# Optimization experiments

Measured on AMD Instinct MI355X. Metric: run time of the kernel, lower is better.

## Reference

```python
import jax, jax.numpy as jnp
import numpy as np

B, C, H, W = 32, 64, 128, 128
RADIUS = 30


def _dw(x, w, dil, pad):
    # depthwise conv, NCHW, groups = C
    return jax.lax.conv_general_dilated(
        x, w, window_strides=(1, 1), padding=[(pad, pad), (pad, pad)],
        rhs_dilation=(dil, dil),
        dimension_numbers=('NCHW', 'OIHW', 'NCHW'),
        feature_group_count=x.shape[1])


def _pw(x, w):
    # 1x1 conv: w is [out_ch, in_ch]
    return jnp.einsum('bchw,oc->bohw', x, w)


def _aff(x, s, b):
    # folded BatchNorm (inference): per-channel scale + bias
    return x * s[None, :, None, None] + b[None, :, None, None]


def setup_inputs() -> dict:
    key = jax.random.key(0)
    ks = iter(jax.random.split(key, 40))
    nk = lambda: next(ks)
    rn = lambda shape, sc=0.1: jax.random.normal(nk(), shape, jnp.float32) * sc
    ru = lambda shape: jax.random.uniform(nk(), shape, jnp.float32, minval=0.5, maxval=1.5)
    d = {'x': jax.random.normal(nk(), (B, C, H, W), jnp.float32)}
    d['dws_dw'] = rn((C, 1, 3, 3)); d['dws_s1'] = ru((C,)); d['dws_b1'] = rn((C,))
    d['dws_pw'] = rn((C, C)); d['dws_s2'] = ru((C,)); d['dws_b2'] = rn((C,))
    kern = {1: 1, 2: 3, 3: 3, 4: 3}
    for i in (1, 2, 3, 4):
        d[f'dw{i}_w'] = rn((C, 1, kern[i], kern[i]))
        d[f'dw{i}_s'] = ru((C,)); d[f'dw{i}_b'] = rn((C,))
        d[f'pw{i}_w'] = rn((C // 4, C)); d[f'pw{i}_s'] = ru((C // 4,)); d[f'pw{i}_b'] = rn((C // 4,))
    d['conv_w'] = rn((1, C)); d['conv_s'] = ru((1,)); d['conv_b'] = rn((1,))
    d['radius'] = RADIUS
    return d


def reference(x, dws_dw, dws_s1, dws_b1, dws_pw, dws_s2, dws_b2,
              dw1_w, dw1_s, dw1_b, pw1_w, pw1_s, pw1_b,
              dw2_w, dw2_s, dw2_b, pw2_w, pw2_s, pw2_b,
              dw3_w, dw3_s, dw3_b, pw3_w, pw3_s, pw3_b,
              dw4_w, dw4_s, dw4_b, pw4_w, pw4_s, pw4_b,
              conv_w, conv_s, conv_b, radius):
    rows, cols = x.shape[-2], x.shape[-1]
    # vectorized radial mask (original builds this with a Python double loop)
    ii = jnp.arange(rows, dtype=jnp.float32)[:, None]
    jj = jnp.arange(cols, dtype=jnp.float32)[None, :]
    dis = jnp.sqrt((ii - rows / 2) ** 2 + (jj - rows / 2) ** 2)  # note: imageSize=rows for both axes, as in original
    mask = (dis < radius).astype(x.dtype)
    # FFT high-pass filter
    xf = jnp.fft.fftshift(jnp.fft.fft2(x, axes=(-2, -1)), axes=(-2, -1))
    hf = xf * (1.0 - mask)
    x_h = jnp.abs(jnp.fft.ifft2(jnp.fft.ifftshift(hf, axes=(-2, -1)), axes=(-2, -1))).astype(x.dtype)
    # DWSConv: depthwise 3x3 + BN + ReLU, then pointwise + BN + ReLU
    e = jax.nn.relu(_aff(_dw(x_h, dws_dw, 1, 1), dws_s1, dws_b1))
    e = jax.nn.relu(_aff(_pw(e, dws_pw), dws_s2, dws_b2))
    skip = e

    def branch(t, dw_w, dw_s, dw_b, pw_w, pw_s, pw_b, dil, pad):
        # DWConv (depthwise + BN + ReLU) then BasicConv2d 1x1 (conv + BN)
        t = jax.nn.relu(_aff(_dw(t, dw_w, dil, pad), dw_s, dw_b))
        return _aff(_pw(t, pw_w), pw_s, pw_b)

    em = jnp.concatenate([
        branch(e, dw1_w, dw1_s, dw1_b, pw1_w, pw1_s, pw1_b, 1, 0),
        branch(e, dw2_w, dw2_s, dw2_b, pw2_w, pw2_s, pw2_b, 1, 1),
        branch(e, dw3_w, dw3_s, dw3_b, pw3_w, pw3_s, pw3_b, 3, 3),
        branch(e, dw4_w, dw4_s, dw4_b, pw4_w, pw4_s, pw4_b, 5, 5),
    ], axis=1) + skip
    edge = jax.nn.relu(_aff(_pw(em, conv_w), conv_s, conv_b))  # [B,1,H,W]
    return _aff(_pw(x + edge, conv_w), conv_s, conv_b)  # shared self.conv applied again
```

## Files before the change

### kernel.cpp

```cpp
#include <hip/hip_runtime.h>


__device__ __forceinline__ float2 cmul(float2 a, float2 b) {
  return make_float2(a.x * b.x - a.y * b.y, a.x * b.y + a.y * b.x);
}
__device__ __forceinline__ float2 cadd(float2 a, float2 b) {
  return make_float2(a.x + b.x, a.y + b.y);
}
__device__ __forceinline__ float2 csub(float2 a, float2 b) {
  return make_float2(a.x - b.x, a.y - b.y);
}
__device__ __forceinline__ float2 conjf2(float2 a) {
  return make_float2(a.x, -a.y);
}

__device__ __forceinline__ void gload16(const float* g, void* l) {
  __builtin_amdgcn_global_load_lds(
      (const __attribute__((address_space(1))) void*)g,
      (__attribute__((address_space(3))) void*)l, 16, 0, 0);
}

__device__ __forceinline__ int swz(int r, int c) {
  return (r << 7) | (c ^ (r & 31));
}

__device__ __forceinline__ void bf3_fwd(float2 x[8], float2 t0, float2 t1,
                                        float2 t2, float2 t3, float2 tp0,
                                        float2 tp1, float2 tpp) {
  float2 y0 = cadd(x[0], x[4]), y4 = cmul(csub(x[0], x[4]), t0);
  float2 y1 = cadd(x[1], x[5]), y5 = cmul(csub(x[1], x[5]), t1);
  float2 y2 = cadd(x[2], x[6]), y6 = cmul(csub(x[2], x[6]), t2);
  float2 y3 = cadd(x[3], x[7]), y7 = cmul(csub(x[3], x[7]), t3);
  float2 z0 = cadd(y0, y2), z2 = cmul(csub(y0, y2), tp0);
  float2 z1 = cadd(y1, y3), z3 = cmul(csub(y1, y3), tp1);
  float2 z4 = cadd(y4, y6), z6 = cmul(csub(y4, y6), tp0);
  float2 z5 = cadd(y5, y7), z7 = cmul(csub(y5, y7), tp1);
  x[0] = cadd(z0, z1); x[1] = cmul(csub(z0, z1), tpp);
  x[2] = cadd(z2, z3); x[3] = cmul(csub(z2, z3), tpp);
  x[4] = cadd(z4, z5); x[5] = cmul(csub(z4, z5), tpp);
  x[6] = cadd(z6, z7); x[7] = cmul(csub(z6, z7), tpp);
}

__device__ __forceinline__ void bf3_inv(float2 x[8], float2 w0, float2 w10,
                                        float2 w11, float2 w20, float2 w21,
                                        float2 w22, float2 w23) {
  float2 t;
  t = cmul(x[1], w0); float2 y0 = cadd(x[0], t), y1 = csub(x[0], t);
  t = cmul(x[3], w0); float2 y2 = cadd(x[2], t), y3 = csub(x[2], t);
  t = cmul(x[5], w0); float2 y4 = cadd(x[4], t), y5 = csub(x[4], t);
  t = cmul(x[7], w0); float2 y6 = cadd(x[6], t), y7 = csub(x[6], t);
  t = cmul(y2, w10); float2 z0 = cadd(y0, t), z2 = csub(y0, t);
  t = cmul(y3, w11); float2 z1 = cadd(y1, t), z3 = csub(y1, t);
  t = cmul(y6, w10); float2 z4 = cadd(y4, t), z6 = csub(y4, t);
  t = cmul(y7, w11); float2 z5 = cadd(y5, t), z7 = csub(y5, t);
  t = cmul(z4, w20); x[0] = cadd(z0, t); x[4] = csub(z0, t);
  t = cmul(z5, w21); x[1] = cadd(z1, t); x[5] = csub(z1, t);
  t = cmul(z6, w22); x[2] = cadd(z2, t); x[6] = csub(z2, t);
  t = cmul(z7, w23); x[3] = cadd(z3, t); x[7] = csub(z3, t);
}

template <bool COL, int S>
__device__ __forceinline__ void fwd_tri(float2* img, const float2* tw,
                                        int tid) {
  constexpr int m4 = 1 << (S - 2);
#pragma unroll
  for (int k = 0; k < 2; ++k) {
    int g = tid + (k << 10);
    int line = COL ? (g & 127) : (g >> 4);
    int gidx = COL ? (g >> 7) : (g & 15);
    int q = gidx >> (S - 2);
    int j = gidx & (m4 - 1);
    int off0 = (q << (S + 1)) + j;
    int ad[8];
    float2 x[8];
#pragma unroll
    for (int i = 0; i < 8; ++i) {
      int el = off0 + i * m4;
      ad[i] = COL ? swz(el, line) : swz(line, el);
      x[i] = img[ad[i]];
    }
    bf3_fwd(x, tw[j << (6 - S)], tw[(j + m4) << (6 - S)],
            tw[(j + 2 * m4) << (6 - S)], tw[(j + 3 * m4) << (6 - S)],
            tw[j << (7 - S)], tw[(j + m4) << (7 - S)], tw[j << (8 - S)]);
#pragma unroll
    for (int i = 0; i < 8; ++i) img[ad[i]] = x[i];
  }
  __syncthreads();
}

__device__ __forceinline__ void fwd_rows6_g(const float* __restrict__ p0,
                                            const float* __restrict__ p1,
                                            float2* img, const float2* tw,
                                            int tid) {
#pragma unroll
  for (int k = 0; k < 2; ++k) {
    int g = tid + (k << 10);
    int line = g >> 4;
    int j = g & 15;
    float2 x[8];
#pragma unroll
    for (int i = 0; i < 8; ++i) {
      int a = (line << 7) + j + (i << 4);
      x[i] = make_float2(p0[a], p1[a]);
    }
    bf3_fwd(x, tw[j], tw[j + 16], tw[j + 32], tw[j + 48], tw[j << 1],
            tw[(j + 16) << 1], tw[j << 2]);
#pragma unroll
    for (int i = 0; i < 8; ++i) img[swz(line, j + (i << 4))] = x[i];
  }
  __syncthreads();
}

__device__ __forceinline__ void fwd_last_rows(float2* img, int tid) {
#pragma unroll
  for (int k = 0; k < 8; ++k) {
    int g = tid + (k << 10);
    int line = g >> 6;
    int pr = g & 63;
    int e0 = pr << 1;
    int a0 = swz(line, e0), a1 = swz(line, e0 + 1);
    float2 a = img[a0], b = img[a1];
    img[a0] = cadd(a, b);
    img[a1] = csub(a, b);
  }
  __syncthreads();
}

__device__ __forceinline__ void fwd_last_cols_mask(float2* img, int tid) {
#pragma unroll
  for (int k = 0; k < 8; ++k) {
    int g = tid + (k << 10);
    int line = g & 127;
    int pr = g >> 7;
    int e0 = pr << 1;
    int a0 = swz(e0, line), a1 = swz(e0 + 1, line);
    float2 a = img[a0], b = img[a1];
    float2 s = cadd(a, b), d = csub(a, b);
    int v = __brev((unsigned)line) >> 25;
    int dv = v - ((v >= 64) << 7);
    int u0 = __brev((unsigned)e0) >> 25;
    int du0 = u0 - ((u0 >= 64) << 7);
    int u1 = __brev((unsigned)(e0 + 1)) >> 25;
    int du1 = u1 - ((u1 >= 64) << 7);
    int dvv = dv * dv;
    img[a0] = (du0 * du0 + dvv < 900) ? make_float2(0.f, 0.f) : s;
    img[a1] = (du1 * du1 + dvv < 900) ? make_float2(0.f, 0.f) : d;
  }
  __syncthreads();
}

template <bool COL, int S>
__device__ __forceinline__ void inv_tri(float2* img, const float2* tw,
                                        int tid) {
  constexpr int m = 1 << S;
#pragma unroll
  for (int k = 0; k < 2; ++k) {
    int g = tid + (k << 10);
    int line = COL ? (g & 127) : (g >> 4);
    int gidx = COL ? (g >> 7) : (g & 15);
    int q = gidx >> S;
    int j = gidx & (m - 1);
    int off0 = (q << (S + 3)) + j;
    int ad[8];
    float2 x[8];
#pragma unroll
    for (int i = 0; i < 8; ++i) {
      int el = off0 + i * m;
      ad[i] = COL ? swz(el, line) : swz(line, el);
      x[i] = img[ad[i]];
    }
    bf3_inv(x, conjf2(tw[j << (6 - S)]), conjf2(tw[j << (5 - S)]),
            conjf2(tw[(j + m) << (5 - S)]), conjf2(tw[j << (4 - S)]),
            conjf2(tw[(j + m) << (4 - S)]), conjf2(tw[(j + 2 * m) << (4 - S)]),
            conjf2(tw[(j + 3 * m) << (4 - S)]));
#pragma unroll
    for (int i = 0; i < 8; ++i) img[ad[i]] = x[i];
  }
  __syncthreads();
}

__device__ __forceinline__ void inv_last_cols(float2* img, const float2* tw,
                                              int tid) {
#pragma unroll
  for (int k = 0; k < 8; ++k) {
    int g = tid + (k << 10);
    int line = g & 127;
    int j = g >> 7;
    int a0 = swz(j, line), a1 = swz(j + 64, line);
    float2 a = img[a0], b = img[a1];
    float2 t = cmul(b, conjf2(tw[j]));
    img[a0] = cadd(a, t);
    img[a1] = csub(a, t);
  }
  __syncthreads();
}

__device__ __forceinline__ void inv_last_rows_store(const float2* img,
                                                    const float2* tw,
                                                    float* __restrict__ q0,
                                                    float* __restrict__ q1,
                                                    int tid) {
#pragma unroll
  for (int k = 0; k < 8; ++k) {
    int g = tid + (k << 10);
    int line = g >> 6;
    int j = g & 63;
    float2 a = img[swz(line, j)], b = img[swz(line, j + 64)];
    float2 t = cmul(b, conjf2(tw[j]));
    float2 o0 = cadd(a, t), o1 = csub(a, t);
    int p = (line << 7) + j;
    q0[p] = fabsf(o0.x) * 6.103515625e-05f;
    q1[p] = fabsf(o0.y) * 6.103515625e-05f;
    q0[p + 64] = fabsf(o1.x) * 6.103515625e-05f;
    q1[p + 64] = fabsf(o1.y) * 6.103515625e-05f;
  }
}

__global__ __launch_bounds__(1024) void k_fft_hp(const float* __restrict__ x,
                                                 float* __restrict__ xh) {
  __shared__ float2 img[16384];
  __shared__ float2 tw[64];
  const int tid = threadIdx.x;
  const size_t base = (size_t)blockIdx.x * 32768;
  const float* p0 = x + base;
  const float* p1 = p0 + 16384;

  if (tid < 64) {
    float ang = -0.04908738521234052f * (float)tid;
    tw[tid] = make_float2(cosf(ang), sinf(ang));
  }
  __syncthreads();

  fwd_rows6_g(p0, p1, img, tw, tid);
  fwd_tri<false, 3>(img, tw, tid);
  fwd_last_rows(img, tid);
  fwd_tri<true, 6>(img, tw, tid);
  fwd_tri<true, 3>(img, tw, tid);
  fwd_last_cols_mask(img, tid);

  inv_tri<true, 0>(img, tw, tid);
  inv_tri<true, 3>(img, tw, tid);
  inv_last_cols(img, tw, tid);
  inv_tri<false, 0>(img, tw, tid);
  inv_tri<false, 3>(img, tw, tid);
  inv_last_rows_store(img, tw, xh + base, xh + base + 16384, tid);
}

#define DWS_G(chunk, buf)                                                      \
  {                                                                            \
    _Pragma("unroll") for (int k2 = 0; k2 < 4; ++k2) {                         \
      int idx = t + (k2 << 8);                                                 \
      if (idx < 800)                                                           \
        gload16(xh + xbase + (size_t)(chunk) * 131072 + offs[k2],              \
                &inT[buf][idx << 2]);                                          \
    }                                                                          \
  }

#define DWS_FIX(buf)                                                           \
  {                                                                            \
    _Pragma("unroll") for (int k2 = 0; k2 < 4; ++k2) {                         \
      if ((fixm >> k2) & 1)                                                    \
        *(float4*)&inT[buf][(t + (k2 << 8)) << 2] =                            \
            make_float4(0.f, 0.f, 0.f, 0.f);                                   \
    }                                                                          \
  }

__global__ __launch_bounds__(256) void k_dws(
    const float* __restrict__ xh, float* __restrict__ e,
    const float* __restrict__ dw_w, const float* __restrict__ s1,
    const float* __restrict__ b1, const float* __restrict__ pw_w,
    const float* __restrict__ s2, const float* __restrict__ b2) {
  __shared__ __align__(16) float inT[2][3200];

  const int t = threadIdx.x;
  const int bb = blockIdx.x >> 6;
  const int ty = (blockIdx.x >> 2) & 15;
  const int tx = blockIdx.x & 3;
  const int r = t >> 5;
  const int x = t & 31;

  const int gy0 = (ty << 3) - 1;
  const int gxb = (tx << 5) - 4;
  const size_t xbase = (size_t)bb << 20;
  const bool bfix = (ty == 0) | (ty == 15) | (tx == 0) | (tx == 3);

  unsigned fixm = 0;
  int offs[4];
#pragma unroll
  for (int k2 = 0; k2 < 4; ++k2) {
    int idx = t + (k2 << 8);
    offs[k2] = 0;
    if (idx < 800) {
      int c = idx / 100;
      int rem = idx - c * 100;
      int row = rem / 10;
      int g = rem - row * 10;
      int grow = gy0 + row;
      int gcol = gxb + (g << 2);
      if ((grow < 0) | (grow > 127) | (gcol < 0) | (gcol > 124))
        fixm |= (1u << k2);
      int grc = grow < 0 ? 0 : (grow > 127 ? 127 : grow);
      int gcc = gcol < 0 ? 0 : (gcol > 124 ? 124 : gcol);
      offs[k2] = (c << 14) + (grc << 7) + gcc;
    }
  }

  float acc[64];
#pragma unroll
  for (int o = 0; o < 64; ++o) acc[o] = 0.f;

  DWS_G(0, 0);
  __syncthreads();

#pragma unroll 1
  for (int chunk = 0; chunk < 8; ++chunk) {
    if (bfix) {
      DWS_FIX(chunk & 1);
      __syncthreads();
    }
    if (chunk < 7) DWS_G(chunk + 1, (chunk + 1) & 1);
    const float* base = &inT[chunk & 1][0];

    float dwv[8];
#pragma unroll
    for (int c = 0; c < 8; ++c) {
      const int cg = (chunk << 3) + c;
      const float* wp = dw_w + cg * 9;
      const float* p = base + c * 400 + r * 40 + x + 3;
      float s = wp[0] * p[0];
      s = fmaf(wp[1], p[1], s);
      s = fmaf(wp[2], p[2], s);
      s = fmaf(wp[3], p[40], s);
      s = fmaf(wp[4], p[41], s);
      s = fmaf(wp[5], p[42], s);
      s = fmaf(wp[6], p[80], s);
      s = fmaf(wp[7], p[81], s);
      s = fmaf(wp[8], p[82], s);
      dwv[c] = fmaxf(fmaf(s, s1[cg], b1[cg]), 0.f);
    }

#pragma unroll
    for (int o = 0; o < 64; ++o) {
      const float* w = pw_w + (o << 6) + (chunk << 3);
#pragma unroll
      for (int c = 0; c < 8; ++c) acc[o] = fmaf(w[c], dwv[c], acc[o]);
    }
    __syncthreads();
  }

  const int gy = (ty << 3) + r;
  const int gx = (tx << 5) + x;
#pragma unroll
  for (int o = 0; o < 64; ++o) {
    float ev = fmaxf(fmaf(acc[o], s2[o], b2[o]), 0.f);
    e[(((size_t)bb * 64 + o) << 14) + (gy << 7) + gx] = ev;
  }
}

struct BrParams {
  const float *dw1w, *dw1s, *dw1b, *pw1w, *pw1s, *pw1b;
  const float *dw2w, *dw2s, *dw2b, *pw2w, *pw2s, *pw2b;
  const float *dw3w, *dw3s, *dw3b, *pw3w, *pw3s, *pw3b;
  const float *dw4w, *dw4s, *dw4b, *pw4w, *pw4s, *pw4b;
};

#define EDGE_G(chunk, buf)                                                     \
  {                                                                            \
    _Pragma("unroll") for (int k2 = 0; k2 < 9; ++k2) {                         \
      int idx = t + (k2 << 8);                                                 \
      if (idx < 2080) {                                                        \
        const float* src = eg + ebase + (size_t)(chunk) * 32768 + eoffs[k2];   \
        if ((fixm >> k2) & 1) src = zp;                  \
        gload16(src, &sE[buf][idx << 2]);                                      \
      }                                                                        \
    }                                                                          \
  }

__global__ __launch_bounds__(256) void k_edge_final(
    const float* __restrict__ eg, const float* __restrict__ xg,
    float* __restrict__ out, BrParams P, const float* __restrict__ cw,
    const float* __restrict__ cs, const float* __restrict__ cb,
    const float* __restrict__ zp) {
  __shared__ __align__(16) float sE[2][8320];
  __shared__ float w2r[768], w3r[768], w4r[768];
  __shared__ float chp[1024];
  __shared__ float dwSs[4][64], dwBs[4][64], gs[4][64];
  __shared__ float dw1Ws[64], cws[64];
  __shared__ float pss[4][16], pbs[4][16];
  __shared__ float KbS, swS;

  const int t = threadIdx.x;
  const int bb = blockIdx.x >> 3;
  const int ty = blockIdx.x & 7;
  const int r = t >> 4;
  const int x0 = (t & 15) << 3;
  const int gy = (ty << 4) + r;
  const int gy0 = (ty << 4) - 5;
  const size_t ebase = (size_t)bb << 20;

  for (int i = t; i < 576; i += 256) {
    int row = i / 9, q = i - row * 9;
    w2r[row * 12 + q] = P.dw2w[i];
    w3r[row * 12 + q] = P.dw3w[i];
    w4r[row * 12 + q] = P.dw4w[i];
  }
  if (t < 64) {
    dw1Ws[t] = P.dw1w[t];
    cws[t] = cw[t];
    dwSs[0][t] = P.dw1s[t]; dwBs[0][t] = P.dw1b[t];
    dwSs[1][t] = P.dw2s[t]; dwBs[1][t] = P.dw2b[t];
    dwSs[2][t] = P.dw3s[t]; dwBs[2][t] = P.dw3b[t];
    dwSs[3][t] = P.dw4s[t]; dwBs[3][t] = P.dw4b[t];
  }
  if (t < 16) {
    pss[0][t] = P.pw1s[t]; pbs[0][t] = P.pw1b[t];
    pss[1][t] = P.pw2s[t]; pbs[1][t] = P.pw2b[t];
    pss[2][t] = P.pw3s[t]; pbs[2][t] = P.pw3b[t];
    pss[3][t] = P.pw4s[t]; pbs[3][t] = P.pw4b[t];
  }
  __syncthreads();
  {
    const int q = t >> 6, c = t & 63;
    const float* pwW = (q == 0) ? P.pw1w : (q == 1) ? P.pw2w
                        : (q == 2) ? P.pw3w : P.pw4w;
    float gv = 0.f;
#pragma unroll
    for (int o = 0; o < 16; ++o)
      gv = fmaf(cws[(q << 4) + o] * pss[q][o], pwW[(o << 6) + c], gv);
    gs[q][c] = gv;
  }
  if (t == 0) {
    float kb = 0.f, sw = 0.f;
#pragma unroll
    for (int i = 0; i < 64; ++i) {
      kb = fmaf(cws[i], pbs[i >> 4][i & 15], kb);
      sw += cws[i];
    }
    KbS = kb;
    swS = sw;
  }
  __syncthreads();
  if (t < 64) {
    float* cp = &chp[t << 4];
    cp[0] = dw1Ws[t];  cp[1] = cws[t];
    cp[2] = dwSs[0][t]; cp[3] = dwBs[0][t];
    cp[4] = dwSs[1][t]; cp[5] = dwBs[1][t];
    cp[6] = dwSs[2][t]; cp[7] = dwBs[2][t];
    cp[8] = dwSs[3][t]; cp[9] = dwBs[3][t];
    cp[10] = gs[0][t]; cp[11] = gs[1][t];
    cp[12] = gs[2][t]; cp[13] = gs[3][t];
  }

  unsigned fixm = 0;
  int eoffs[9];
#pragma unroll
  for (int k2 = 0; k2 < 9; ++k2) {
    int idx = t + (k2 << 8);
    eoffs[k2] = 0;
    if (idx < 2080) {
      int jj = idx >= 1040;
      int rem = idx - (jj ? 1040 : 0);
      int row = rem / 40;
      int q = rem - row * 40;
      int s = q ^ (q >> 3);
      int grow = gy0 + row;
      if ((grow < 0) | (grow > 127) | (s < 2) | (s > 33)) fixm |= (1u << k2);
      int grc = grow < 0 ? 0 : (grow > 127 ? 127 : grow);
      int sc = s < 2 ? 2 : (s > 33 ? 33 : s);
      eoffs[k2] = (jj << 14) + (grc << 7) + (sc << 2) - 8;
    }
  }

  const int gbase = (t & 15) << 1;
  int so[6];
#pragma unroll
  for (int k = 0; k < 6; ++k) {
    int g = gbase + k;
    so[k] = (g ^ (g >> 3)) << 2;
  }

  EDGE_G(0, 0);
  __syncthreads();

  float eacc[8], es8[8], sxa[8];
#pragma unroll
  for (int k = 0; k < 8; ++k) { eacc[k] = 0.f; es8[k] = 0.f; sxa[k] = 0.f; }

  const float csv = cs[0], cbv = cb[0];

#pragma unroll 1
  for (int c = 0; c < 32; ++c) {
    if (c + 1 < 32) EDGE_G(c + 1, (c + 1) & 1);
    const float* bp = &sE[c & 1][0];
#pragma unroll 1
    for (int j = 0; j < 2; ++j) {
      const int cg = (c << 1) + j;
      const float* ldc = bp + j * 4160;
      const float* xp = xg + (((size_t)bb * 64 + cg) << 14) + (gy << 7) + x0;
      float xv[8];
      *(float4*)&xv[0] = *(const float4*)xp;
      *(float4*)&xv[4] = *(const float4*)(xp + 4);
      const float4 Q0 = *(const float4*)&chp[cg << 4];
      const float4 Q1 = *(const float4*)&chp[(cg << 4) + 4];
      const float4 Q2 = *(const float4*)&chp[(cg << 4) + 8];
      const float4 Q3 = *(const float4*)&chp[(cg << 4) + 12];

      float cr[24];
      const float* rowc = ldc + (r + 5) * 160;
      *(float4*)&cr[0] = *(const float4*)(rowc + so[0]);
      *(float4*)&cr[4] = *(const float4*)(rowc + so[1]);
      *(float4*)&cr[8] = *(const float4*)(rowc + so[2]);
      *(float4*)&cr[12] = *(const float4*)(rowc + so[3]);
      *(float4*)&cr[16] = *(const float4*)(rowc + so[4]);
      *(float4*)&cr[20] = *(const float4*)(rowc + so[5]);

#pragma unroll
      for (int k = 0; k < 8; ++k) {
        float ec = cr[8 + k];
        es8[k] = fmaf(Q0.y, ec, es8[k]);
        float d0 = fmaxf(fmaf(ec * Q0.x, Q0.z, Q0.w), 0.f);
        eacc[k] = fmaf(Q2.z, d0, eacc[k]);
      }
      float mm[24], pp[24];
      {
        const float4 w2a = *(const float4*)&w2r[cg * 12];
        const float4 w2b = *(const float4*)&w2r[cg * 12 + 4];
        const float4 w2c = *(const float4*)&w2r[cg * 12 + 8];
        const float* rm = ldc + (r + 4) * 160;
        const float* rp = ldc + (r + 6) * 160;
        *(float4*)&mm[0] = *(const float4*)(rm + so[1]);
        *(float4*)&mm[4] = *(const float4*)(rm + so[2]);
        *(float4*)&mm[8] = *(const float4*)(rm + so[3]);
        *(float4*)&mm[12] = *(const float4*)(rm + so[4]);
        *(float4*)&pp[0] = *(const float4*)(rp + so[1]);
        *(float4*)&pp[4] = *(const float4*)(rp + so[2]);
        *(float4*)&pp[8] = *(const float4*)(rp + so[3]);
        *(float4*)&pp[12] = *(const float4*)(rp + so[4]);
#pragma unroll
        for (int k = 0; k < 8; ++k) {
          float s = w2a.x * mm[3 + k];
          s = fmaf(w2a.y, mm[4 + k], s);
          s = fmaf(w2a.z, mm[5 + k], s);
          s = fmaf(w2a.w, cr[7 + k], s);
          s = fmaf(w2b.x, cr[8 + k], s);
          s = fmaf(w2b.y, cr[9 + k], s);
          s = fmaf(w2b.z, pp[3 + k], s);
          s = fmaf(w2b.w, pp[4 + k], s);
          s = fmaf(w2c.x, pp[5 + k], s);
          float d1 = fmaxf(fmaf(s, Q1.x, Q1.y), 0.f);
          eacc[k] = fmaf(Q2.w, d1, eacc[k]);
        }
      }
      {
        const float4 w3a = *(const float4*)&w3r[cg * 12];
        const float4 w3b = *(const float4*)&w3r[cg * 12 + 4];
        const float4 w3c = *(const float4*)&w3r[cg * 12 + 8];
        const float* rm = ldc + (r + 2) * 160;
        const float* rp = ldc + (r + 8) * 160;
        *(float4*)&mm[0] = *(const float4*)(rm + so[1]);
        *(float4*)&mm[4] = *(const float4*)(rm + so[2]);
        *(float4*)&mm[8] = *(const float4*)(rm + so[3]);
        *(float4*)&mm[12] = *(const float4*)(rm + so[4]);
        *(float4*)&pp[0] = *(const float4*)(rp + so[1]);
        *(float4*)&pp[4] = *(const float4*)(rp + so[2]);
        *(float4*)&pp[8] = *(const float4*)(rp + so[3]);
        *(float4*)&pp[12] = *(const float4*)(rp + so[4]);
#pragma unroll
        for (int k = 0; k < 8; ++k) {
          float s = w3a.x * mm[1 + k];
          s = fmaf(w3a.y, mm[4 + k], s);
          s = fmaf(w3a.z, mm[7 + k], s);
          s = fmaf(w3a.w, cr[5 + k], s);
          s = fmaf(w3b.x, cr[8 + k], s);
          s = fmaf(w3b.y, cr[11 + k], s);
          s = fmaf(w3b.z, pp[1 + k], s);
          s = fmaf(w3b.w, pp[4 + k], s);
          s = fmaf(w3c.x, pp[7 + k], s);
          float d2 = fmaxf(fmaf(s, Q1.z, Q1.w), 0.f);
          eacc[k] = fmaf(Q3.x, d2, eacc[k]);
        }
      }
      {
        const float4 w4a = *(const float4*)&w4r[cg * 12];
        const float4 w4b = *(const float4*)&w4r[cg * 12 + 4];
        const float4 w4c = *(const float4*)&w4r[cg * 12 + 8];
        const float* rm = ldc + (r + 0) * 160;
        const float* rp = ldc + (r + 10) * 160;
        *(float4*)&mm[0] = *(const float4*)(rm + so[0]);
        *(float4*)&mm[4] = *(const float4*)(rm + so[1]);
        *(float4*)&mm[8] = *(const float4*)(rm + so[2]);
        *(float4*)&mm[12] = *(const float4*)(rm + so[3]);
        *(float4*)&mm[16] = *(const float4*)(rm + so[4]);
        *(float4*)&mm[20] = *(const float4*)(rm + so[5]);
        *(float4*)&pp[0] = *(const float4*)(rp + so[0]);
        *(float4*)&pp[4] = *(const float4*)(rp + so[1]);
        *(float4*)&pp[8] = *(const float4*)(rp + so[2]);
        *(float4*)&pp[12] = *(const float4*)(rp + so[3]);
        *(float4*)&pp[16] = *(const float4*)(rp + so[4]);
        *(float4*)&pp[20] = *(const float4*)(rp + so[5]);
#pragma unroll
        for (int k = 0; k < 8; ++k) {
          float s = w4a.x * mm[3 + k];
          s = fmaf(w4a.y, mm[8 + k], s);
          s = fmaf(w4a.z, mm[13 + k], s);
          s = fmaf(w4a.w, cr[3 + k], s);
          s = fmaf(w4b.x, cr[8 + k], s);
          s = fmaf(w4b.y, cr[13 + k], s);
          s = fmaf(w4b.z, pp[3 + k], s);
          s = fmaf(w4b.w, pp[8 + k], s);
          s = fmaf(w4c.x, pp[13 + k], s);
          float d3 = fmaxf(fmaf(s, Q2.x, Q2.y), 0.f);
          eacc[k] = fmaf(Q3.y, d3, eacc[k]);
        }
      }
#pragma unroll
      for (int k = 0; k < 8; ++k) sxa[k] = fmaf(Q0.y, xv[k], sxa[k]);
    }
    __syncthreads();
  }

  const float kb = KbS, sw = swS;
  float ov[8];
#pragma unroll
  for (int k = 0; k < 8; ++k) {
    float ee = fmaxf(fmaf(eacc[k] + kb + es8[k], csv, cbv), 0.f);
    ov[k] = fmaf(sxa[k] + ee * sw, csv, cbv);
  }
  float* op = out + ((size_t)bb << 14) + (gy << 7) + x0;
  *(float4*)op = *(float4*)&ov[0];
  *(float4*)(op + 4) = *(float4*)&ov[4];
}

extern "C" void kernel_launch(void* const* d_in, const int* in_sizes, int n_in,
                              void* d_out, int out_size, void* d_ws,
                              size_t ws_size, hipStream_t stream) {
  (void)in_sizes; (void)n_in; (void)out_size; (void)ws_size;
  const float* x = (const float*)d_in[0];
  const float* dws_dw = (const float*)d_in[1];
  const float* dws_s1 = (const float*)d_in[2];
  const float* dws_b1 = (const float*)d_in[3];
  const float* dws_pw = (const float*)d_in[4];
  const float* dws_s2 = (const float*)d_in[5];
  const float* dws_b2 = (const float*)d_in[6];
  BrParams P;
  P.dw1w = (const float*)d_in[7];  P.dw1s = (const float*)d_in[8];
  P.dw1b = (const float*)d_in[9];  P.pw1w = (const float*)d_in[10];
  P.pw1s = (const float*)d_in[11]; P.pw1b = (const float*)d_in[12];
  P.dw2w = (const float*)d_in[13]; P.dw2s = (const float*)d_in[14];
  P.dw2b = (const float*)d_in[15]; P.pw2w = (const float*)d_in[16];
  P.pw2s = (const float*)d_in[17]; P.pw2b = (const float*)d_in[18];
  P.dw3w = (const float*)d_in[19]; P.dw3s = (const float*)d_in[20];
  P.dw3b = (const float*)d_in[21]; P.pw3w = (const float*)d_in[22];
  P.pw3s = (const float*)d_in[23]; P.pw3b = (const float*)d_in[24];
  P.dw4w = (const float*)d_in[25]; P.dw4s = (const float*)d_in[26];
  P.dw4b = (const float*)d_in[27]; P.pw4w = (const float*)d_in[28];
  P.pw4s = (const float*)d_in[29]; P.pw4b = (const float*)d_in[30];
  const float* conv_w = (const float*)d_in[31];
  const float* conv_s = (const float*)d_in[32];
  const float* conv_b = (const float*)d_in[33];

  float* xh = (float*)d_ws;
  float* e = xh + (size_t)33554432;

  hipLaunchKernelGGL(k_fft_hp, dim3(1024), dim3(1024), 0, stream, x, xh);
  hipLaunchKernelGGL(k_dws, dim3(2048), dim3(256), 0, stream, xh, e, dws_dw,
                     dws_s1, dws_b1, dws_pw, dws_s2, dws_b2);
  hipMemsetAsync(xh, 0, 4096, stream);
  hipLaunchKernelGGL(k_edge_final, dim3(256), dim3(256), 0, stream, e, x,
                     (float*)d_out, P, conv_w, conv_s, conv_b,
                     (const float*)xh);
}
```

Baseline: 616.5 us.

## Triple-buffer DWS input tiles with finer chunks and manual waitcnt barriers

Reworks the depthwise-separable stage's LDS staging from a double buffer of 8-channel chunks to a triple buffer of 4-channel chunks. Loads are issued two chunks ahead and each iteration ends with explicit vmcnt/lgkmcnt waits and a single raw barrier, replacing the extra syncthreads around the border zero-fix. This is meant to hide global-load latency and reduce barrier count. It also changes the FFT LDS swizzle to XOR in higher column bits to cut bank conflicts. The hand-written waitcnt counts must match the loads in flight, and padded slots now load dummy data.

Result: slower. 680.9 us (+10.4%).

```diff
diff --git a/kernel.cpp b/kernel.cpp
--- a/kernel.cpp
+++ b/kernel.cpp
@@ -21,7 +21,7 @@
 }
 
 __device__ __forceinline__ int swz(int r, int c) {
-  return (r << 7) | (c ^ (r & 31));
+  return (r << 7) | ((c ^ (c >> 4)) ^ (r & 31));
 }
 
 __device__ __forceinline__ void bf3_fwd(float2 x[8], float2 t0, float2 t1,
@@ -248,17 +248,16 @@
 
 #define DWS_G(chunk, buf)                                                      \
   {                                                                            \
-    _Pragma("unroll") for (int k2 = 0; k2 < 4; ++k2) {                         \
+    _Pragma("unroll") for (int k2 = 0; k2 < 2; ++k2) {                         \
       int idx = t + (k2 << 8);                                                 \
-      if (idx < 800)                                                           \
-        gload16(xh + xbase + (size_t)(chunk) * 131072 + offs[k2],              \
-                &inT[buf][idx << 2]);                                          \
+      gload16(xh + xbase + (size_t)(chunk) * 65536 + offs[k2],                 \
+              &inT[buf][idx << 2]);                                            \
     }                                                                          \
   }
 
 #define DWS_FIX(buf)                                                           \
   {                                                                            \
-    _Pragma("unroll") for (int k2 = 0; k2 < 4; ++k2) {                         \
+    _Pragma("unroll") for (int k2 = 0; k2 < 2; ++k2) {                         \
       if ((fixm >> k2) & 1)                                                    \
         *(float4*)&inT[buf][(t + (k2 << 8)) << 2] =                            \
             make_float4(0.f, 0.f, 0.f, 0.f);                                   \
@@ -270,7 +269,7 @@
     const float* __restrict__ dw_w, const float* __restrict__ s1,
     const float* __restrict__ b1, const float* __restrict__ pw_w,
     const float* __restrict__ s2, const float* __restrict__ b2) {
-  __shared__ __align__(16) float inT[2][3200];
+  __shared__ __align__(16) float inT[3][2048];
 
   const int t = threadIdx.x;
   const int bb = blockIdx.x >> 6;
@@ -285,16 +284,15 @@
   const bool bfix = (ty == 0) | (ty == 15) | (tx == 0) | (tx == 3);
 
   unsigned fixm = 0;
-  int offs[4];
-#pragma unroll
-  for (int k2 = 0; k2 < 4; ++k2) {
+  int offs[2];
+#pragma unroll
+  for (int k2 = 0; k2 < 2; ++k2) {
     int idx = t + (k2 << 8);
-    offs[k2] = 0;
-    if (idx < 800) {
-      int c = idx / 100;
-      int rem = idx - c * 100;
-      int row = rem / 10;
-      int g = rem - row * 10;
+    int c = idx >> 7;
+    int within = idx & 127;
+    if (within < 100) {
+      int row = within / 10;
+      int g = within - row * 10;
       int grow = gy0 + row;
       int gcol = gxb + (g << 2);
       if ((grow < 0) | (grow > 127) | (gcol < 0) | (gcol > 124))
@@ -302,6 +300,8 @@
       int grc = grow < 0 ? 0 : (grow > 127 ? 127 : grow);
       int gcc = gcol < 0 ? 0 : (gcol > 124 ? 124 : gcol);
       offs[k2] = (c << 14) + (grc << 7) + gcc;
+    } else {
+      offs[k2] = (within - 100) << 2;
     }
   }
 
@@ -310,23 +310,24 @@
   for (int o = 0; o < 64; ++o) acc[o] = 0.f;
 
   DWS_G(0, 0);
-  __syncthreads();
+  DWS_G(1, 1);
+  asm volatile("s_waitcnt vmcnt(2)" ::: "memory");
+  if (bfix) DWS_FIX(0);
+  asm volatile("s_waitcnt lgkmcnt(0)" ::: "memory");
+  __builtin_amdgcn_s_barrier();
+  __builtin_amdgcn_sched_barrier(0);
 
 #pragma unroll 1
-  for (int chunk = 0; chunk < 8; ++chunk) {
-    if (bfix) {
-      DWS_FIX(chunk & 1);
-      __syncthreads();
-    }
-    if (chunk < 7) DWS_G(chunk + 1, (chunk + 1) & 1);
-    const float* base = &inT[chunk & 1][0];
-
-    float dwv[8];
-#pragma unroll
-    for (int c = 0; c < 8; ++c) {
-      const int cg = (chunk << 3) + c;
+  for (int chunk = 0; chunk < 16; ++chunk) {
+    if (chunk + 2 < 16) DWS_G(chunk + 2, (chunk + 2) % 3);
+    const float* base = &inT[chunk % 3][0];
+
+    float dwv[4];
+#pragma unroll
+    for (int c = 0; c < 4; ++c) {
+      const int cg = (chunk << 2) + c;
       const float* wp = dw_w + cg * 9;
-      const float* p = base + c * 400 + r * 40 + x + 3;
+      const float* p = base + c * 512 + r * 40 + x + 3;
       float s = wp[0] * p[0];
       s = fmaf(wp[1], p[1], s);
       s = fmaf(wp[2], p[2], s);
@@ -341,11 +342,20 @@
 
 #pragma unroll
     for (int o = 0; o < 64; ++o) {
-      const float* w = pw_w + (o << 6) + (chunk << 3);
-#pragma unroll
-      for (int c = 0; c < 8; ++c) acc[o] = fmaf(w[c], dwv[c], acc[o]);
-    }
-    __syncthreads();
+      const float* w = pw_w + (o << 6) + (chunk << 2);
+#pragma unroll
+      for (int c = 0; c < 4; ++c) acc[o] = fmaf(w[c], dwv[c], acc[o]);
+    }
+
+    if (chunk < 14) {
+      asm volatile("s_waitcnt vmcnt(2)" ::: "memory");
+    } else {
+      asm volatile("s_waitcnt vmcnt(0)" ::: "memory");
+    }
+    if (bfix && chunk + 1 < 16) DWS_FIX((chunk + 1) % 3);
+    asm volatile("s_waitcnt lgkmcnt(0)" ::: "memory");
+    __builtin_amdgcn_s_barrier();
+    __builtin_amdgcn_sched_barrier(0);
   }
 
   const int gy = (ty << 3) + r;
```
